# Performance work log

Measured on AMD Instinct MI355X. Metric: run time of the kernel, lower is better.

Reference implementation:

```python
import jax, jax.numpy as jnp
import numpy as np

T, IN, H, OUT, L = 2048, 128, 128, 128, 2


def setup_inputs() -> dict:
    key = jax.random.key(0)
    ks = jax.random.split(key, 12)
    s_in = 1.0 / np.sqrt(IN)
    s_h = 1.0 / np.sqrt(H)
    s_ff = 1.0 / np.sqrt(2 * H)
    return {
        "emb": jax.random.normal(ks[0], (T, IN), jnp.float32),
        "start": jax.random.randint(ks[1], (T,), 0, 2).astype(jnp.int32),
        "w_in": jax.random.normal(ks[2], (H, IN), jnp.float32) * s_in,
        "b_in": jnp.zeros((H,), jnp.float32),
        "w_out": jax.random.normal(ks[3], (OUT, H), jnp.float32) * s_h,
        "b_out": jnp.zeros((OUT,), jnp.float32),
        "w_f": jax.random.normal(ks[4], (L, 1, H), jnp.float32) * s_h,
        "b_f": jnp.zeros((L, 1), jnp.float32),
        "w_i": jax.random.normal(ks[5], (L, 1, H), jnp.float32) * s_h,
        "b_i": jnp.zeros((L, 1), jnp.float32),
        "w_v": jax.random.normal(ks[6], (L, H, H), jnp.float32) * s_h,
        "b_v": jnp.zeros((L, H), jnp.float32),
        "w_q": jax.random.normal(ks[7], (L, H, H), jnp.float32) * s_h,
        "b_q": jnp.zeros((L, H), jnp.float32),
        "w_k": jax.random.normal(ks[8], (L, H, H), jnp.float32) * s_h,
        "b_k": jnp.zeros((L, H), jnp.float32),
        "w_o": jax.random.normal(ks[9], (L, H, H), jnp.float32) * s_h,
        "b_o": jnp.zeros((L, H), jnp.float32),
        "w_ff": jax.random.normal(ks[10], (L, H, 2 * H), jnp.float32) * s_ff,
        "b_ff": jnp.zeros((L, H), jnp.float32),
    }


def _mlstm_layer(x, gate_mask, w_f, b_f, w_i, b_i, w_v, b_v, w_q, b_q, w_k, b_k, w_o, b_o):
    # x: [T, H] layer input; gate_mask: [T] (0.0 at episode starts -> reset)
    Hdim = x.shape[-1]
    i = jnp.exp(x @ w_i.T + b_i)                           # [T, 1] exp input gate
    v = x @ w_v.T + b_v                                    # [T, H]
    k = (x * (1.0 / np.sqrt(Hdim))) @ w_k.T + b_k          # [T, H] (1/sqrt(H) applied before Linear)
    C = i[:, :, None] * (v[:, :, None] * k[:, None, :])    # [T, H, H] gated outer products
    n = i * k                                              # [T, H]
    g = jax.nn.sigmoid(x @ w_f.T + b_f)[:, 0] * gate_mask  # [T] forget gate, zeroed at resets

    def step(carry, inp):
        S, m = carry
        Ct, nt, gt = inp
        S = gt * S + Ct
        m = gt * m + nt
        return (S, m), (S, m)

    init = (jnp.zeros((Hdim, Hdim), x.dtype), jnp.zeros((Hdim,), x.dtype))
    _, (S_all, m_all) = jax.lax.scan(step, init, (C, n, g))  # [T,H,H], [T,H]

    q = x @ w_q.T + b_q                                    # [T, H]
    o = jax.nn.sigmoid(x @ w_o.T + b_o)                    # [T, H]
    num = jnp.einsum('thk,tk->th', S_all, q)               # C @ q per step
    den = jnp.maximum(jnp.abs(jnp.einsum('th,th->t', m_all, q))[:, None], 1.0)
    return o * (num / den)


def reference(emb, start, w_in, b_in, w_out, b_out, w_f, b_f, w_i, b_i,
              w_v, b_v, w_q, b_q, w_k, b_k, w_o, b_o, w_ff, b_ff):
    gate_mask = 1.0 - start.astype(emb.dtype)              # reset => discard previous state
    e = emb @ w_in.T + b_in                                # [T, H]
    z = e
    for l in range(w_f.shape[0]):
        h = _mlstm_layer(z, gate_mask, w_f[l], b_f[l], w_i[l], b_i[l],
                         w_v[l], b_v[l], w_q[l], b_q[l], w_k[l], b_k[l], w_o[l], b_o[l])
        z = jax.nn.leaky_relu(jnp.concatenate([h, e], axis=-1) @ w_ff[l].T + b_ff[l])
    return z @ w_out.T + b_out
```

## Files before the change

kernel.cpp:

```cpp
#include <hip/hip_runtime.h>
#include <math.h>

#define TT 2048
#define HH 128
#define ROWS 8
#define SP 132
#define XR 144
#define NBLK (TT / ROWS)

__device__ __forceinline__ float dot4(float4 a, float4 b) {
    return a.x * b.x + a.y * b.y + a.z * b.z + a.w * b.w;
}

__device__ __forceinline__ int xidx(int r, int k) {
    return r * XR + ((k >> 5) * 36) + (k & 31);
}

__device__ __forceinline__ float2 load_f2_agent(const float* p) {
    unsigned long long u = __hip_atomic_load((const unsigned long long*)p,
                                             __ATOMIC_RELAXED, __HIP_MEMORY_SCOPE_AGENT);
    float2 r;
    r.x = __uint_as_float((unsigned)(u & 0xffffffffull));
    r.y = __uint_as_float((unsigned)(u >> 32));
    return r;
}
__device__ __forceinline__ float load_f_agent(const float* p) {
    return __hip_atomic_load(p, __ATOMIC_RELAXED, __HIP_MEMORY_SCOPE_AGENT);
}
__device__ __forceinline__ void store_f_agent(float* p, float v) {
    __hip_atomic_store(p, v, __ATOMIC_RELAXED, __HIP_MEMORY_SCOPE_AGENT);
}

__global__ __launch_bounds__(256) void prep_kernel(
        const float* __restrict__ w_in, const float* __restrict__ w_out,
        const float* __restrict__ w_v, const float* __restrict__ w_q,
        const float* __restrict__ w_k, const float* __restrict__ w_o,
        const float* __restrict__ w_ff,
        float4* __restrict__ win_p, float4* __restrict__ wout_p,
        float4* __restrict__ wcat, float4* __restrict__ wff_p,
        unsigned* __restrict__ bar) {
    int i = blockIdx.x * 256 + threadIdx.x;
    if (blockIdx.x == 0 && threadIdx.x < 16) bar[threadIdx.x] = 0u;
    if (i < 4096) {
        int cg = i >> 7, col = i & 127;
        win_p[i] = ((const float4*)w_in)[col * 32 + cg];
    } else if (i < 8192) {
        int j = i - 4096, cg = j >> 7, col = j & 127;
        wout_p[j] = ((const float4*)w_out)[col * 32 + cg];
    } else if (i < 40960) {
        int j = i - 8192;
        int l = j >> 14, r = j & 16383, cg = r >> 9, col = r & 511;
        int sel = col >> 7, cm = col & 127;
        const float* s = (sel == 0 ? w_v : sel == 1 ? w_q : sel == 2 ? w_k : w_o) + l * HH * HH;
        wcat[j] = ((const float4*)s)[cm * 32 + cg];
    } else {
        int j = i - 40960;
        int l = j >> 13, r = j & 8191, cg = r >> 7, col = r & 127;
        const float* s = w_ff + l * HH * 256;
        wff_p[j] = ((const float4*)s)[col * 64 + cg];
    }
}

__device__ __forceinline__ void grid_barrier(unsigned* __restrict__ ctr) {
    __syncthreads();
    if (threadIdx.x == 0) {
        atomicAdd(ctr, 1u);
        while (__hip_atomic_load(ctr, __ATOMIC_RELAXED, __HIP_MEMORY_SCOPE_AGENT)
               < (unsigned)NBLK) {
            __builtin_amdgcn_s_sleep(8);
        }
    }
    __syncthreads();
}

__device__ __forceinline__ void stage_wsh(const float4* __restrict__ src, float4* lds) {
    int tid = threadIdx.x;
    int wv = tid >> 6;
#pragma unroll
    for (int it = 0; it < 16; ++it) {
        __builtin_amdgcn_global_load_lds(
            (const __attribute__((address_space(1))) unsigned int*)(src + it * 512 + tid),
            (__attribute__((address_space(3))) unsigned int*)(lds + it * 512 + wv * 64),
            16, 0, 0);
    }
}

__device__ __forceinline__ void attn_row(int t0,
        const float* __restrict__ kb, const float* __restrict__ vb,
        const float* __restrict__ qs, const float* __restrict__ os,
        const float* __restrict__ g, const float* __restrict__ iexp,
        float* __restrict__ hs) {
    int tid = threadIdx.x;
    int wv = tid >> 6, lane = tid & 63;
    int t = t0 + wv;
    float2 q2 = *(const float2*)(qs + wv * SP + 2 * lane);
    float2 o2 = *(const float2*)(os + wv * SP + 2 * lane);
    int tp = t;
    float2 k2 = load_f2_agent(kb + tp * HH + 2 * lane);
    float2 v2 = load_f2_agent(vb + tp * HH + 2 * lane);
    float ie = load_f_agent(iexp + tp), gv = load_f_agent(g + tp);
    float nx = 0.f, ny = 0.f, dsum = 0.f, decay = 1.f;
    while (true) {
        bool cont = (tp > 0) && (gv != 0.f);
        float2 k2n = {0.f, 0.f}, v2n = {0.f, 0.f};
        float ien = 0.f, gvn = 0.f;
        if (cont) {
            k2n = load_f2_agent(kb + (tp - 1) * HH + 2 * lane);
            v2n = load_f2_agent(vb + (tp - 1) * HH + 2 * lane);
            ien = load_f_agent(iexp + tp - 1); gvn = load_f_agent(g + tp - 1);
        }
        float p = k2.x * q2.x + k2.y * q2.y;
#pragma unroll
        for (int off = 1; off <= 32; off <<= 1) p += __shfl_xor(p, off, 64);
        float coeff = decay * ie * p;
        nx += coeff * v2.x; ny += coeff * v2.y; dsum += coeff;
        if (!cont) break;
        decay *= gv;
        tp--; k2 = k2n; v2 = v2n; ie = ien; gv = gvn;
    }
    float inv = 1.f / fmaxf(fabsf(dsum), 1.f);
    int d = 2 * lane;
    *(float2*)(hs + wv * XR + (d >> 5) * 36 + (d & 31)) =
        make_float2(o2.x * nx * inv, o2.y * ny * inv);
}

__device__ __forceinline__ void proj_fi(int t0, const float* __restrict__ xls,
        const float* __restrict__ w_f, const float* __restrict__ b_f,
        const float* __restrict__ w_i, const float* __restrict__ b_i,
        const int* __restrict__ start, float* __restrict__ g, float* __restrict__ iexp) {
    int tid = threadIdx.x;
    int wv = tid >> 6, lane = tid & 63;
    int d = 2 * lane;
    float2 xv = *(const float2*)(xls + wv * XR + (d >> 5) * 36 + (d & 31));
    float pf = xv.x * w_f[d] + xv.y * w_f[d + 1];
    float pi = xv.x * w_i[d] + xv.y * w_i[d + 1];
#pragma unroll
    for (int off = 1; off <= 32; off <<= 1) {
        pf += __shfl_xor(pf, off, 64);
        pi += __shfl_xor(pi, off, 64);
    }
    if (lane == 0) {
        int t = t0 + wv;
        store_f_agent(g + t, start[t] ? 0.f : 1.f / (1.f + expf(-(pf + b_f[0]))));
        store_f_agent(iexp + t, expf(pi + b_i[0]));
    }
}

__device__ __forceinline__ void proj_block(int t0, const float* __restrict__ xls,
        const float4* __restrict__ wc,
        const float* __restrict__ b_v, const float* __restrict__ b_q,
        const float* __restrict__ b_k, const float* __restrict__ b_o,
        float* __restrict__ kb, float* __restrict__ vb,
        float* __restrict__ qs, float* __restrict__ os) {
    int tid = threadIdx.x;
    int lane = tid & 63, wv = tid >> 6;
    int kc = lane >> 4, c = lane & 15;
    int cslot = wv * 16 + c;
    float accv[8] = {}, accq[8] = {}, acck[8] = {}, acco[8] = {};
#pragma unroll
    for (int j = 0; j < 8; ++j) {
        const float4* wb = wc + (kc * 8 + j) * 512;
        float4 w0 = wb[cslot];
        float4 w1 = wb[128 + cslot];
        float4 w2 = wb[256 + cslot];
        float4 w3 = wb[384 + cslot];
#pragma unroll
        for (int rr = 0; rr < 8; ++rr) {
            float4 x4 = *(const float4*)(xls + rr * XR + kc * 36 + 4 * j);
            accv[rr] += dot4(x4, w0);
            accq[rr] += dot4(x4, w1);
            acck[rr] += dot4(x4, w2);
            acco[rr] += dot4(x4, w3);
        }
    }
#pragma unroll
    for (int rr = 0; rr < 8; ++rr) {
        accv[rr] += __shfl_xor(accv[rr], 16, 64); accv[rr] += __shfl_xor(accv[rr], 32, 64);
        accq[rr] += __shfl_xor(accq[rr], 16, 64); accq[rr] += __shfl_xor(accq[rr], 32, 64);
        acck[rr] += __shfl_xor(acck[rr], 16, 64); acck[rr] += __shfl_xor(acck[rr], 32, 64);
        acco[rr] += __shfl_xor(acco[rr], 16, 64); acco[rr] += __shfl_xor(acco[rr], 32, 64);
    }
    if (kc == 0) {
        const float ks = 0.088388347648318447f;
        float bv = b_v[cslot], bq = b_q[cslot], bk = b_k[cslot], bo = b_o[cslot];
#pragma unroll
        for (int rr = 0; rr < 8; ++rr) {
            int t = t0 + rr;
            store_f_agent(vb + t * HH + cslot, accv[rr] + bv);
            qs[rr * SP + cslot] = accq[rr] + bq;
            store_f_agent(kb + t * HH + cslot, acck[rr] * ks + bk);
            os[rr * SP + cslot] = 1.f / (1.f + expf(-(acco[rr] + bo)));
        }
    }
}

__device__ __forceinline__ void ff_block(const float* __restrict__ hsb,
        const float* __restrict__ esb, const float4* wffl,
        const float* __restrict__ b_ff, float* __restrict__ zs) {
    int tid = threadIdx.x;
    int lane = tid & 63, wv = tid >> 6;
    int kc = lane >> 3, c = lane & 7;
    int cslot = wv * 8 + c;
    const float* xb = (kc < 4) ? hsb : esb;
    int coff = (kc & 3) * 36;
    float a0[8] = {}, a1[8] = {};
#pragma unroll
    for (int j = 0; j < 8; ++j) {
        const float4* wl = wffl + (kc * 8 + j) * 128;
        float4 w0 = wl[cslot];
        float4 w1 = wl[64 + cslot];
#pragma unroll
        for (int rr = 0; rr < 8; ++rr) {
            float4 x4 = *(const float4*)(xb + rr * XR + coff + 4 * j);
            a0[rr] += dot4(x4, w0);
            a1[rr] += dot4(x4, w1);
        }
    }
#pragma unroll
    for (int rr = 0; rr < 8; ++rr) {
        a0[rr] += __shfl_xor(a0[rr], 8, 64); a0[rr] += __shfl_xor(a0[rr], 16, 64);
        a0[rr] += __shfl_xor(a0[rr], 32, 64);
        a1[rr] += __shfl_xor(a1[rr], 8, 64); a1[rr] += __shfl_xor(a1[rr], 16, 64);
        a1[rr] += __shfl_xor(a1[rr], 32, 64);
    }
    if (kc == 0) {
        float b0 = b_ff[cslot], b1 = b_ff[cslot + 64];
#pragma unroll
        for (int rr = 0; rr < 8; ++rr) {
            float z0 = a0[rr] + b0, z1 = a1[rr] + b1;
            z0 = z0 > 0.f ? z0 : 0.01f * z0;
            z1 = z1 > 0.f ? z1 : 0.01f * z1;
            zs[xidx(rr, cslot)] = z0;
            zs[xidx(rr, cslot + 64)] = z1;
        }
    }
}

__device__ __forceinline__ void dense128(int t0, const float* __restrict__ xls,
        const float4* __restrict__ Wp, const float* __restrict__ b,
        float* __restrict__ yg, float* __restrict__ ys) {
    int tid = threadIdx.x;
    int lane = tid & 63, wv = tid >> 6;
    int kc = lane >> 3, c = lane & 7;
    int cslot = wv * 8 + c;
    float a0[8] = {}, a1[8] = {};
#pragma unroll
    for (int j = 0; j < 4; ++j) {
        float4 w0 = Wp[(kc * 4 + j) * 128 + cslot];
        float4 w1 = Wp[(kc * 4 + j) * 128 + 64 + cslot];
        int off = (kc >> 1) * 36 + (kc & 1) * 16 + 4 * j;
#pragma unroll
        for (int rr = 0; rr < 8; ++rr) {
            float4 x4 = *(const float4*)(xls + rr * XR + off);
            a0[rr] += dot4(x4, w0);
            a1[rr] += dot4(x4, w1);
        }
    }
#pragma unroll
    for (int rr = 0; rr < 8; ++rr) {
        a0[rr] += __shfl_xor(a0[rr], 8, 64); a0[rr] += __shfl_xor(a0[rr], 16, 64);
        a0[rr] += __shfl_xor(a0[rr], 32, 64);
        a1[rr] += __shfl_xor(a1[rr], 8, 64); a1[rr] += __shfl_xor(a1[rr], 16, 64);
        a1[rr] += __shfl_xor(a1[rr], 32, 64);
    }
    if (kc == 0) {
        float b0 = b[cslot], b1 = b[cslot + 64];
#pragma unroll
        for (int rr = 0; rr < 8; ++rr) {
            float y0 = a0[rr] + b0, y1 = a1[rr] + b1;
            if (ys) { ys[xidx(rr, cslot)] = y0; ys[xidx(rr, cslot + 64)] = y1; }
            if (yg) {
                yg[(t0 + rr) * HH + cslot] = y0;
                yg[(t0 + rr) * HH + cslot + 64] = y1;
            }
        }
    }
}

__global__ __launch_bounds__(512, 2) void mega_kernel(
        const float* __restrict__ emb, const int* __restrict__ start,
        const float4* __restrict__ win_p, const float* __restrict__ b_in,
        const float4* __restrict__ wcat,
        const float* __restrict__ b_v, const float* __restrict__ b_q,
        const float* __restrict__ b_k, const float* __restrict__ b_o,
        const float* __restrict__ w_f, const float* __restrict__ b_f,
        const float* __restrict__ w_i, const float* __restrict__ b_i,
        const float4* __restrict__ wff_p, const float* __restrict__ b_ff,
        const float4* __restrict__ wout_p, const float* __restrict__ b_out,
        float* __restrict__ k0b, float* __restrict__ v0b,
        float* __restrict__ k1b, float* __restrict__ v1b,
        float* __restrict__ g0, float* __restrict__ i0,
        float* __restrict__ g1, float* __restrict__ i1,
        unsigned* __restrict__ bar,
        float* __restrict__ out) {
    __shared__ float xs[ROWS * XR];
    __shared__ float es[ROWS * XR];
    __shared__ float hs[ROWS * XR];
    __shared__ float zs[ROWS * XR];
    __shared__ float qs[ROWS * SP];
    __shared__ float os[ROWS * SP];
    __shared__ float4 wsh[8192];
    int tid = threadIdx.x;
    int t0 = blockIdx.x * ROWS;
    int wv = tid >> 6, lane = tid & 63;
    int d = 2 * lane;

    float2 ev = *(const float2*)(emb + (t0 + wv) * HH + d);
    *(float2*)(xs + wv * XR + (d >> 5) * 36 + (d & 31)) = ev;
    __syncthreads();
    dense128(t0, xs, win_p, b_in, (float*)0, es);
    __syncthreads();
    proj_block(t0, es, wcat, b_v, b_q, b_k, b_o, k0b, v0b, qs, os);
    proj_fi(t0, es, w_f, b_f, w_i, b_i, start, g0, i0);
    grid_barrier(bar + 0);

    stage_wsh(wff_p, wsh);
    attn_row(t0, k0b, v0b, qs, os, g0, i0, hs);
    __syncthreads();
    ff_block(hs, es, wsh, b_ff, zs);
    __syncthreads();
    proj_block(t0, zs, wcat + 16384, b_v + HH, b_q + HH, b_k + HH, b_o + HH,
               k1b, v1b, qs, os);
    proj_fi(t0, zs, w_f + HH, b_f + 1, w_i + HH, b_i + 1, start, g1, i1);
    grid_barrier(bar + 1);

    stage_wsh(wff_p + 8192, wsh);
    attn_row(t0, k1b, v1b, qs, os, g1, i1, hs);
    __syncthreads();
    ff_block(hs, es, wsh, b_ff + HH, zs);
    __syncthreads();
    dense128(t0, zs, wout_p, b_out, out, (float*)0);
}

extern "C" void kernel_launch(void* const* d_in, const int* in_sizes, int n_in,
                              void* d_out, int out_size, void* d_ws, size_t ws_size,
                              hipStream_t stream) {
    const float* emb   = (const float*)d_in[0];
    const int*   start = (const int*)  d_in[1];
    const float* w_in  = (const float*)d_in[2];
    const float* b_in  = (const float*)d_in[3];
    const float* w_out = (const float*)d_in[4];
    const float* b_out = (const float*)d_in[5];
    const float* w_f   = (const float*)d_in[6];
    const float* b_f   = (const float*)d_in[7];
    const float* w_i   = (const float*)d_in[8];
    const float* b_i   = (const float*)d_in[9];
    const float* w_v   = (const float*)d_in[10];
    const float* b_v   = (const float*)d_in[11];
    const float* w_q   = (const float*)d_in[12];
    const float* b_q   = (const float*)d_in[13];
    const float* w_k   = (const float*)d_in[14];
    const float* b_k   = (const float*)d_in[15];
    const float* w_o   = (const float*)d_in[16];
    const float* b_o   = (const float*)d_in[17];
    const float* w_ff  = (const float*)d_in[18];
    const float* b_ff  = (const float*)d_in[19];
    float* out = (float*)d_out;

    unsigned* bar = (unsigned*)d_ws;
    float* ws = (float*)d_ws + 64;
    float* k0b = ws; ws += TT * HH;
    float* v0b = ws; ws += TT * HH;
    float* k1b = ws; ws += TT * HH;
    float* v1b = ws; ws += TT * HH;
    float* g0  = ws; ws += TT;
    float* i0  = ws; ws += TT;
    float* g1  = ws; ws += TT;
    float* i1  = ws; ws += TT;
    float4* win_p  = (float4*)ws; ws += 16384;
    float4* wout_p = (float4*)ws; ws += 16384;
    float4* wcat   = (float4*)ws; ws += 131072;
    float4* wff_p  = (float4*)ws; ws += 65536;

    prep_kernel<<<dim3(224), dim3(256), 0, stream>>>(
        w_in, w_out, w_v, w_q, w_k, w_o, w_ff, win_p, wout_p, wcat, wff_p, bar);
    mega_kernel<<<dim3(NBLK), dim3(512), 0, stream>>>(
        emb, start, win_p, b_in, wcat,
        b_v, b_q, b_k, b_o, w_f, b_f, w_i, b_i,
        wff_p, b_ff, wout_p, b_out,
        k0b, v0b, k1b, v1b, g0, i0, g1, i1,
        bar, out);
}
```

Measured before the change: 145.4 us.

## Double block size to 1024 threads and split projection columns across wave halves

Launches the mega kernel with 1024 threads per block instead of 512. The dense, FF and QKVO projection loops are repartitioned so each wave computes half as many output columns, which cuts per-thread accumulator registers. The attention and gate routines are limited to the first 8 waves. The goal is more parallel work and latency hiding per block, at the cost of idle waves during the serial attention phase and heavier __syncthreads and grid barriers across 16 waves.

Result: faster. 141.7 us (-2.6%).

```diff
diff --git a/kernel.cpp b/kernel.cpp
--- a/kernel.cpp
+++ b/kernel.cpp
@@ -77,10 +77,10 @@
     int tid = threadIdx.x;
     int wv = tid >> 6;
 #pragma unroll
-    for (int it = 0; it < 16; ++it) {
+    for (int it = 0; it < 8; ++it) {
         __builtin_amdgcn_global_load_lds(
-            (const __attribute__((address_space(1))) unsigned int*)(src + it * 512 + tid),
-            (__attribute__((address_space(3))) unsigned int*)(lds + it * 512 + wv * 64),
+            (const __attribute__((address_space(1))) unsigned int*)(src + it * 1024 + tid),
+            (__attribute__((address_space(3))) unsigned int*)(lds + it * 1024 + wv * 64),
             16, 0, 0);
     }
 }
@@ -92,6 +92,7 @@
         float* __restrict__ hs) {
     int tid = threadIdx.x;
     int wv = tid >> 6, lane = tid & 63;
+    if (wv >= 8) return;
     int t = t0 + wv;
     float2 q2 = *(const float2*)(qs + wv * SP + 2 * lane);
     float2 o2 = *(const float2*)(os + wv * SP + 2 * lane);
@@ -130,6 +131,7 @@
         const int* __restrict__ start, float* __restrict__ g, float* __restrict__ iexp) {
     int tid = threadIdx.x;
     int wv = tid >> 6, lane = tid & 63;
+    if (wv >= 8) return;
     int d = 2 * lane;
     float2 xv = *(const float2*)(xls + wv * XR + (d >> 5) * 36 + (d & 31));
     float pf = xv.x * w_f[d] + xv.y * w_f[d + 1];
@@ -153,43 +155,44 @@
         float* __restrict__ kb, float* __restrict__ vb,
         float* __restrict__ qs, float* __restrict__ os) {
     int tid = threadIdx.x;
-    int lane = tid & 63, wv = tid >> 6;
+    int lane = tid & 63, w = tid >> 6;
     int kc = lane >> 4, c = lane & 15;
-    int cslot = wv * 16 + c;
-    float accv[8] = {}, accq[8] = {}, acck[8] = {}, acco[8] = {};
+    int cslot = (w & 7) * 16 + c;
+    int mp = w >> 3;
+    float a0[8] = {}, a1[8] = {};
 #pragma unroll
     for (int j = 0; j < 8; ++j) {
-        const float4* wb = wc + (kc * 8 + j) * 512;
+        const float4* wb = wc + (kc * 8 + j) * 512 + mp * 256;
         float4 w0 = wb[cslot];
         float4 w1 = wb[128 + cslot];
-        float4 w2 = wb[256 + cslot];
-        float4 w3 = wb[384 + cslot];
 #pragma unroll
         for (int rr = 0; rr < 8; ++rr) {
             float4 x4 = *(const float4*)(xls + rr * XR + kc * 36 + 4 * j);
-            accv[rr] += dot4(x4, w0);
-            accq[rr] += dot4(x4, w1);
-            acck[rr] += dot4(x4, w2);
-            acco[rr] += dot4(x4, w3);
+            a0[rr] += dot4(x4, w0);
+            a1[rr] += dot4(x4, w1);
         }
     }
 #pragma unroll
     for (int rr = 0; rr < 8; ++rr) {
-        accv[rr] += __shfl_xor(accv[rr], 16, 64); accv[rr] += __shfl_xor(accv[rr], 32, 64);
-        accq[rr] += __shfl_xor(accq[rr], 16, 64); accq[rr] += __shfl_xor(accq[rr], 32, 64);
-        acck[rr] += __shfl_xor(acck[rr], 16, 64); acck[rr] += __shfl_xor(acck[rr], 32, 64);
-        acco[rr] += __shfl_xor(acco[rr], 16, 64); acco[rr] += __shfl_xor(acco[rr], 32, 64);
+        a0[rr] += __shfl_xor(a0[rr], 16, 64); a0[rr] += __shfl_xor(a0[rr], 32, 64);
+        a1[rr] += __shfl_xor(a1[rr], 16, 64); a1[rr] += __shfl_xor(a1[rr], 32, 64);
     }
     if (kc == 0) {
-        const float ks = 0.088388347648318447f;
-        float bv = b_v[cslot], bq = b_q[cslot], bk = b_k[cslot], bo = b_o[cslot];
-#pragma unroll
-        for (int rr = 0; rr < 8; ++rr) {
-            int t = t0 + rr;
-            store_f_agent(vb + t * HH + cslot, accv[rr] + bv);
-            qs[rr * SP + cslot] = accq[rr] + bq;
-            store_f_agent(kb + t * HH + cslot, acck[rr] * ks + bk);
-            os[rr * SP + cslot] = 1.f / (1.f + expf(-(acco[rr] + bo)));
+        if (mp == 0) {
+            float bv = b_v[cslot], bq = b_q[cslot];
+#pragma unroll
+            for (int rr = 0; rr < 8; ++rr) {
+                store_f_agent(vb + (t0 + rr) * HH + cslot, a0[rr] + bv);
+                qs[rr * SP + cslot] = a1[rr] + bq;
+            }
+        } else {
+            const float ks = 0.088388347648318447f;
+            float bk = b_k[cslot], bo = b_o[cslot];
+#pragma unroll
+            for (int rr = 0; rr < 8; ++rr) {
+                store_f_agent(kb + (t0 + rr) * HH + cslot, a0[rr] * ks + bk);
+                os[rr * SP + cslot] = 1.f / (1.f + expf(-(a1[rr] + bo)));
+            }
         }
     }
 }
@@ -198,40 +201,34 @@
         const float* __restrict__ esb, const float4* wffl,
         const float* __restrict__ b_ff, float* __restrict__ zs) {
     int tid = threadIdx.x;
-    int lane = tid & 63, wv = tid >> 6;
+    int lane = tid & 63, w = tid >> 6;
     int kc = lane >> 3, c = lane & 7;
-    int cslot = wv * 8 + c;
+    int col = (w >> 3) * 64 + (w & 7) * 8 + c;
     const float* xb = (kc < 4) ? hsb : esb;
     int coff = (kc & 3) * 36;
-    float a0[8] = {}, a1[8] = {};
+    float a0[8] = {};
 #pragma unroll
     for (int j = 0; j < 8; ++j) {
-        const float4* wl = wffl + (kc * 8 + j) * 128;
-        float4 w0 = wl[cslot];
-        float4 w1 = wl[64 + cslot];
+        float4 w0 = wffl[(kc * 8 + j) * 128 + col];
 #pragma unroll
         for (int rr = 0; rr < 8; ++rr) {
             float4 x4 = *(const float4*)(xb + rr * XR + coff + 4 * j);
             a0[rr] += dot4(x4, w0);
-            a1[rr] += dot4(x4, w1);
         }
     }
 #pragma unroll
     for (int rr = 0; rr < 8; ++rr) {
-        a0[rr] += __shfl_xor(a0[rr], 8, 64); a0[rr] += __shfl_xor(a0[rr], 16, 64);
+        a0[rr] += __shfl_xor(a0[rr], 8, 64);
+        a0[rr] += __shfl_xor(a0[rr], 16, 64);
         a0[rr] += __shfl_xor(a0[rr], 32, 64);
-        a1[rr] += __shfl_xor(a1[rr], 8, 64); a1[rr] += __shfl_xor(a1[rr], 16, 64);
-        a1[rr] += __shfl_xor(a1[rr], 32, 64);
     }
     if (kc == 0) {
-        float b0 = b_ff[cslot], b1 = b_ff[cslot + 64];
-#pragma unroll
-        for (int rr = 0; rr < 8; ++rr) {
-            float z0 = a0[rr] + b0, z1 = a1[rr] + b1;
-            z0 = z0 > 0.f ? z0 : 0.01f * z0;
-            z1 = z1 > 0.f ? z1 : 0.01f * z1;
-            zs[xidx(rr, cslot)] = z0;
-            zs[xidx(rr, cslot + 64)] = z1;
+        float bb = b_ff[col];
+#pragma unroll
+        for (int rr = 0; rr < 8; ++rr) {
+            float z = a0[rr] + bb;
+            z = z > 0.f ? z : 0.01f * z;
+            zs[xidx(rr, col)] = z;
         }
     }
 }
@@ -240,44 +237,38 @@
         const float4* __restrict__ Wp, const float* __restrict__ b,
         float* __restrict__ yg, float* __restrict__ ys) {
     int tid = threadIdx.x;
-    int lane = tid & 63, wv = tid >> 6;
+    int lane = tid & 63, w = tid >> 6;
     int kc = lane >> 3, c = lane & 7;
-    int cslot = wv * 8 + c;
-    float a0[8] = {}, a1[8] = {};
+    int col = (w >> 3) * 64 + (w & 7) * 8 + c;
+    float a0[8] = {};
 #pragma unroll
     for (int j = 0; j < 4; ++j) {
-        float4 w0 = Wp[(kc * 4 + j) * 128 + cslot];
-        float4 w1 = Wp[(kc * 4 + j) * 128 + 64 + cslot];
+        float4 w0 = Wp[(kc * 4 + j) * 128 + col];
         int off = (kc >> 1) * 36 + (kc & 1) * 16 + 4 * j;
 #pragma unroll
         for (int rr = 0; rr < 8; ++rr) {
             float4 x4 = *(const float4*)(xls + rr * XR + off);
             a0[rr] += dot4(x4, w0);
-            a1[rr] += dot4(x4, w1);
         }
     }
 #pragma unroll
     for (int rr = 0; rr < 8; ++rr) {
-        a0[rr] += __shfl_xor(a0[rr], 8, 64); a0[rr] += __shfl_xor(a0[rr], 16, 64);
+        a0[rr] += __shfl_xor(a0[rr], 8, 64);
+        a0[rr] += __shfl_xor(a0[rr], 16, 64);
         a0[rr] += __shfl_xor(a0[rr], 32, 64);
-        a1[rr] += __shfl_xor(a1[rr], 8, 64); a1[rr] += __shfl_xor(a1[rr], 16, 64);
-        a1[rr] += __shfl_xor(a1[rr], 32, 64);
     }
     if (kc == 0) {
-        float b0 = b[cslot], b1 = b[cslot + 64];
-#pragma unroll
-        for (int rr = 0; rr < 8; ++rr) {
-            float y0 = a0[rr] + b0, y1 = a1[rr] + b1;
-            if (ys) { ys[xidx(rr, cslot)] = y0; ys[xidx(rr, cslot + 64)] = y1; }
-            if (yg) {
-                yg[(t0 + rr) * HH + cslot] = y0;
-                yg[(t0 + rr) * HH + cslot + 64] = y1;
-            }
-        }
-    }
-}
-
-__global__ __launch_bounds__(512, 2) void mega_kernel(
+        float bb = b[col];
+#pragma unroll
+        for (int rr = 0; rr < 8; ++rr) {
+            float y = a0[rr] + bb;
+            if (ys) ys[xidx(rr, col)] = y;
+            if (yg) yg[(t0 + rr) * HH + col] = y;
+        }
+    }
+}
+
+__global__ __launch_bounds__(1024, 4) void mega_kernel(
         const float* __restrict__ emb, const int* __restrict__ start,
         const float4* __restrict__ win_p, const float* __restrict__ b_in,
         const float4* __restrict__ wcat,
@@ -302,11 +293,11 @@
     __shared__ float4 wsh[8192];
     int tid = threadIdx.x;
     int t0 = blockIdx.x * ROWS;
-    int wv = tid >> 6, lane = tid & 63;
-    int d = 2 * lane;
-
-    float2 ev = *(const float2*)(emb + (t0 + wv) * HH + d);
-    *(float2*)(xs + wv * XR + (d >> 5) * 36 + (d & 31)) = ev;
+
+    {
+        int row = tid >> 7, dd = tid & 127;
+        xs[row * XR + (dd >> 5) * 36 + (dd & 31)] = emb[(t0 + row) * HH + dd];
+    }
     __syncthreads();
     dense128(t0, xs, win_p, b_in, (float*)0, es);
     __syncthreads();
@@ -374,7 +365,7 @@
 
     prep_kernel<<<dim3(224), dim3(256), 0, stream>>>(
         w_in, w_out, w_v, w_q, w_k, w_o, w_ff, win_p, wout_p, wcat, wff_p, bar);
-    mega_kernel<<<dim3(NBLK), dim3(512), 0, stream>>>(
+    mega_kernel<<<dim3(NBLK), dim3(1024), 0, stream>>>(
         emb, start, win_p, b_in, wcat,
         b_v, b_q, b_k, b_o, w_f, b_f, w_i, b_i,
         wff_p, b_ff, wout_p, b_out,
```
